# Optimization experiments

Measured on AMD Instinct MI355X. Metric: run time of the kernel, lower is better.

Reference implementation:

```python
import jax, jax.numpy as jnp
import numpy as np

B = 1024
EMB_DIM = 128      # channels fed to VQ; each channel's 5*5=25 spatial vector is one token
CODEBOOK = 1024
COMMIT = 0.25


def conv2d(x, w, b, pad=1):
    y = jax.lax.conv_general_dilated(x, w, (1, 1), [(pad, pad), (pad, pad)],
                                     dimension_numbers=('NCHW', 'OIHW', 'NCHW'))
    return y + b[None, :, None, None]


def maxpool2x2(x):
    b, c, h, w = x.shape
    xr = x.reshape(b, c, h // 2, 2, w // 2, 2).transpose(0, 1, 2, 4, 3, 5).reshape(b, c, h // 2, w // 2, 4)
    return jnp.max(xr, axis=-1), jnp.argmax(xr, axis=-1)


def maxunpool2x2(x, idx):
    b, c, h, w = x.shape
    y = x[..., None] * jax.nn.one_hot(idx, 4, dtype=x.dtype)
    return y.reshape(b, c, h, w, 2, 2).transpose(0, 1, 2, 4, 3, 5).reshape(b, c, h * 2, w * 2)


def setup_inputs() -> dict:
    key = jax.random.key(0)
    ks = jax.random.split(key, 12)
    f32 = jnp.float32

    def he(k, shape, fan_in):
        return jax.random.normal(k, shape, f32) * (2.0 / fan_in) ** 0.5

    return {
        'x': jax.random.normal(ks[0], (B, 3, 20, 20), f32),
        'enc1_w': he(ks[1], (32, 3, 3, 3), 27), 'enc1_b': jnp.zeros((32,), f32),
        'enc2_w': he(ks[2], (96, 32, 3, 3), 288), 'enc2_b': jnp.zeros((96,), f32),
        'pre_w': he(ks[3], (EMB_DIM, 96, 1, 1), 96), 'pre_b': jnp.zeros((EMB_DIM,), f32),
        'codebook': jax.random.normal(ks[4], (CODEBOOK, 25), f32),
        'trans_w': he(ks[5], (EMB_DIM, 96, 1, 1), EMB_DIM), 'trans_b': jnp.zeros((96,), f32),
        'dec1_w': he(ks[6], (32, 96, 3, 3), 864), 'dec1_b': jnp.zeros((32,), f32),
        'dec2_w': he(ks[7], (3, 32, 3, 3), 288), 'dec2_b': jnp.zeros((3,), f32),
        'hpe_w1': he(ks[8], (2400, 32), 2400), 'hpe_b1': jnp.zeros((32,), f32),
        'hpe_w2': he(ks[9], (32, 36), 32), 'hpe_b2': jnp.zeros((36,), f32),
    }


def reference(x, enc1_w, enc1_b, enc2_w, enc2_b, pre_w, pre_b, codebook,
              trans_w, trans_b, dec1_w, dec1_b, dec2_w, dec2_b,
              hpe_w1, hpe_b1, hpe_w2, hpe_b2):
    bsz = x.shape[0]
    # ---- Encoder: conv+relu+pool x2, keeping pool argmax indices ----
    h1 = jax.nn.relu(conv2d(x, enc1_w, enc1_b))          # [B,32,20,20]
    p1, idx1 = maxpool2x2(h1)                            # [B,32,10,10]
    h2 = jax.nn.relu(conv2d(p1, enc2_w, enc2_b))         # [B,96,10,10]
    z, idx2 = maxpool2x2(h2)                             # [B,96,5,5]
    # ---- pre-VQ 1x1 conv, tokens are per-channel 25-dim spatial vectors ----
    vq = conv2d(z, pre_w, pre_b, pad=0).reshape(bsz, -1, 25)   # [B,EMB_DIM,25]
    flat = vq.reshape(-1, 25)
    # squared L2 distances to codebook, argmin quantization
    d = (jnp.sum(flat * flat, -1, keepdims=True)
         - 2.0 * flat @ codebook.T
         + jnp.sum(codebook * codebook, -1))             # [B*EMB_DIM, CODEBOOK]
    indices = jnp.argmin(d, axis=-1).reshape(bsz, -1)    # [B,EMB_DIM]
    quantized = codebook[indices]                        # [B,EMB_DIM,25] gather
    vq_loss = COMMIT * jnp.mean((jax.lax.stop_gradient(quantized) - vq) ** 2)
    # unreliable_mode == 2 -> noisy_indices = indices (identity path)
    z_rec = codebook[indices].reshape(bsz, -1, 5, 5)     # [B,EMB_DIM,5,5]
    # ---- ConvTranspose2d 1x1 (torch weight layout [in,out,1,1]) ----
    latent = jnp.einsum('bihw,io->bohw', z_rec, trans_w[:, :, 0, 0]) + trans_b[None, :, None, None]
    # ---- Decoder: unpool(idx2)+conv+relu, unpool(idx1)+conv ----
    u2 = maxunpool2x2(latent, idx2)                      # [B,96,10,10]
    d1 = jax.nn.relu(conv2d(u2, dec1_w, dec1_b))         # [B,32,10,10]
    u1 = maxunpool2x2(d1, idx1)                          # [B,32,20,20]
    r_x = conv2d(u1, dec2_w, dec2_b)                     # [B,3,20,20]
    # ---- pose head on flattened latent (2400 = 96*5*5) ----
    feat = latent.reshape(bsz, -1)
    kp = jax.nn.relu(feat @ hpe_w1 + hpe_b1) @ hpe_w2 + hpe_b2
    return vq_loss, r_x, kp.reshape(bsz, -1, 2)
```

## Files before the change

kernel.cpp:

```cpp
#include <hip/hip_runtime.h>

typedef unsigned char u8;
typedef unsigned long long u64;
typedef _Float16 h2 __attribute__((ext_vector_type(2)));

__device__ inline h2 h2bits(unsigned int u) { union { unsigned int u; h2 h; } c; c.u = u; return c.h; }
__device__ inline unsigned int bitsh2(h2 h) { union { unsigned int u; h2 h; } c; c.h = h; return c.u; }
__device__ inline unsigned int f2hbits(float v) {
    union { _Float16 h; unsigned short u; } c; c.h = (_Float16)v; return (unsigned int)c.u;
}

#if __has_builtin(__builtin_amdgcn_fdot2)
__device__ inline float fdot2(h2 a, h2 b, float c) { return __builtin_amdgcn_fdot2(a, b, c, false); }
#else
__device__ inline float fdot2(h2 a, h2 b, float c) {
    return c + (float)a.x * (float)b.x + (float)a.y * (float)b.y;
}
#endif

__global__ __launch_bounds__(256) void k0t(const float* __restrict__ cb,
                                           float* __restrict__ cnorm,
                                           float* __restrict__ lossacc,
                                           const float* __restrict__ e2w,
                                           float* __restrict__ wT2,
                                           const float* __restrict__ d1w,
                                           unsigned int* __restrict__ wH6u) {
    int g = blockIdx.x * 256 + threadIdx.x;
    if (g < 1024) {
        float s = 0.f;
#pragma unroll
        for (int d = 0; d < 25; ++d) { float v = cb[g * 25 + d]; s += v * v; }
        cnorm[g] = s;
    }
    if (g == 0) lossacc[0] = 0.f;
    for (int i = g; i < 27648; i += 8192) {
        int oc = i / 288, r = i % 288, ci = r / 9, k = r % 9;
        wT2[((ci * 3 + k / 3) * 96 + oc) * 3 + (k % 3)] = e2w[i];
    }
    for (int i = g; i < 13824; i += 8192) {
        int oc = i & 31, r = i >> 5;
        int kx = r % 3, r2 = r / 3, ky = r2 % 3, cp = r2 / 3;
        float a = d1w[(oc * 96 + 2 * cp) * 9 + ky * 3 + kx];
        float b = d1w[(oc * 96 + 2 * cp + 1) * 9 + ky * 3 + kx];
        h2 v; v.x = (_Float16)a; v.y = (_Float16)b;
        wH6u[i] = bitsh2(v);
    }
}

__global__ __launch_bounds__(128) void k1_enc1(const float* __restrict__ x,
                                               const float* __restrict__ w,
                                               const float* __restrict__ bias,
                                               float* __restrict__ p1,
                                               u64* __restrict__ idx1p) {
    const int img = blockIdx.x;
    const int tid = threadIdx.x;
    __shared__ __align__(16) float xs[1320];
    __shared__ float wss[864];
    __shared__ float bss[32];
    for (int i = tid; i < 1320; i += 128) xs[i] = 0.f;
    for (int i = tid; i < 864; i += 128) wss[i] = w[i];
    if (tid < 32) bss[tid] = bias[tid];
    __syncthreads();
    for (int i = tid; i < 1200; i += 128) {
        int ci = i / 400, s = i % 400, y = s / 20, xx = s % 20;
        xs[ci * 440 + y * 22 + xx + 1] = x[img * 1200 + i];
    }
    __syncthreads();
    if (tid >= 100) return;
    const int r = tid / 10, c = tid % 10;
    int ry[4]; bool mv[4];
#pragma unroll
    for (int wy = 0; wy < 4; ++wy) {
        int yy = 2 * r - 1 + wy;
        mv[wy] = (yy >= 0) && (yy <= 19);
        ry[wy] = min(max(yy, 0), 19);
    }
    u64 idxbits = 0;
    for (int ocg = 0; ocg < 4; ++ocg) {
        float acc[8][4];
#pragma unroll
        for (int j = 0; j < 8; ++j) {
            float bb = bss[ocg * 8 + j];
#pragma unroll
            for (int q = 0; q < 4; ++q) acc[j][q] = bb;
        }
        for (int ci = 0; ci < 3; ++ci) {
            float win[4][4];
#pragma unroll
            for (int wy = 0; wy < 4; ++wy)
#pragma unroll
                for (int wx = 0; wx < 4; ++wx) {
                    float v = xs[ci * 440 + ry[wy] * 22 + 2 * c + wx];
                    win[wy][wx] = mv[wy] ? v : 0.f;
                }
#pragma unroll
            for (int j = 0; j < 8; ++j) {
                const float* wr = &wss[((ocg * 8 + j) * 3 + ci) * 9];
#pragma unroll
                for (int q = 0; q < 4; ++q) {
                    int dr = q >> 1, dc = q & 1;
#pragma unroll
                    for (int ky = 0; ky < 3; ++ky)
#pragma unroll
                        for (int kx = 0; kx < 3; ++kx)
                            acc[j][q] = fmaf(win[dr + ky][dc + kx], wr[ky * 3 + kx], acc[j][q]);
                }
            }
        }
#pragma unroll
        for (int j = 0; j < 8; ++j) {
            int oc = ocg * 8 + j;
            float best = -1.f; int bi = 0;
#pragma unroll
            for (int q = 0; q < 4; ++q) {
                float v = fmaxf(acc[j][q], 0.f);
                if (v > best) { best = v; bi = q; }
            }
            p1[img * 3200 + oc * 100 + tid] = best;
            idxbits |= (u64)bi << (2 * oc);
        }
    }
    idx1p[img * 100 + tid] = idxbits;
}

__global__ __launch_bounds__(256) void k2_enc2(const float* __restrict__ p1,
                                               const float* __restrict__ wT2,
                                               const float* __restrict__ bias,
                                               float* __restrict__ z_g,
                                               u8* __restrict__ idx2) {
    const int img = blockIdx.x;
    const int tid = threadIdx.x;
    __shared__ __align__(16) float up[4608];
    __shared__ __align__(16) float wch[6912];
    for (int i = tid; i < 4608; i += 256) up[i] = 0.f;
    __syncthreads();
    for (int i = tid; i < 3200; i += 256) {
        int ci = i / 100, s = i % 100;
        up[ci * 144 + (s / 10 + 1) * 12 + (s % 10) + 1] = p1[img * 3200 + i];
    }
    const int wv = tid >> 6;
    const int l  = tid & 63;
    const int ocsub = (l >= 25) ? 1 : 0;
    const int pos = l - ocsub * 25;
    const bool act = (l < 50);
    const int oc0 = wv * 24 + ocsub * 12;
    const int r = pos / 5, c = pos % 5;
    float acc[12][4];
#pragma unroll
    for (int j = 0; j < 12; ++j)
#pragma unroll
        for (int q = 0; q < 4; ++q) acc[j][q] = 0.f;
    for (int chunk = 0; chunk < 4; ++chunk) {
        __syncthreads();
        for (int i = tid; i < 6912; i += 256) wch[i] = wT2[chunk * 6912 + i];
        __syncthreads();
        if (act) {
            for (int cil = 0; cil < 8; ++cil) {
                const int base = (chunk * 8 + cil) * 144;
                float win[4][4];
#pragma unroll
                for (int wy = 0; wy < 4; ++wy) {
                    float2 a = *(const float2*)&up[base + (2 * r + wy) * 12 + 2 * c];
                    float2 b = *(const float2*)&up[base + (2 * r + wy) * 12 + 2 * c + 2];
                    win[wy][0] = a.x; win[wy][1] = a.y; win[wy][2] = b.x; win[wy][3] = b.y;
                }
#pragma unroll
                for (int ky = 0; ky < 3; ++ky) {
                    const float* wk = &wch[(cil * 3 + ky) * 288 + oc0 * 3];
                    float wreg[36];
#pragma unroll
                    for (int i4 = 0; i4 < 9; ++i4)
                        *(float4*)(wreg + 4 * i4) = *(const float4*)(wk + 4 * i4);
#pragma unroll
                    for (int j = 0; j < 12; ++j)
#pragma unroll
                        for (int q = 0; q < 4; ++q) {
                            int dr = q >> 1, dc = q & 1;
#pragma unroll
                            for (int kx = 0; kx < 3; ++kx)
                                acc[j][q] = fmaf(win[dr + ky][dc + kx], wreg[j * 3 + kx], acc[j][q]);
                        }
                }
            }
        }
    }
    if (act) {
#pragma unroll
        for (int j = 0; j < 12; ++j) {
            int oc = oc0 + j;
            float bb = bias[oc];
            float best = -1.f; int bi = 0;
#pragma unroll
            for (int q = 0; q < 4; ++q) {
                float v = fmaxf(acc[j][q] + bb, 0.f);
                if (v > best) { best = v; bi = q; }
            }
            z_g[img * 2400 + oc * 25 + pos] = best;
            idx2[img * 2400 + oc * 25 + pos] = (u8)bi;
        }
    }
}

__global__ __launch_bounds__(128) void k3a_pre(const float* __restrict__ z_g,
                                               const float* __restrict__ w,
                                               const float* __restrict__ bias,
                                               float* __restrict__ vqb) {
    const int img = blockIdx.x;
    const int tid = threadIdx.x;
    __shared__ __align__(16) float zs[2688];
    __shared__ float ob[3200];
    for (int i = tid; i < 2688; i += 128) zs[i] = 0.f;
    __syncthreads();
    for (int i = tid; i < 2400; i += 128)
        zs[(i / 25) * 28 + (i % 25)] = z_g[img * 2400 + i];
    __syncthreads();
    float acc[25];
    {
        float bbv = bias[tid];
#pragma unroll
        for (int s = 0; s < 25; ++s) acc[s] = bbv;
    }
    const float4* w4 = (const float4*)(w + tid * 96);
    for (int c4 = 0; c4 < 24; ++c4) {
        float4 wv = w4[c4];
        const int ci = c4 * 4;
#pragma unroll
        for (int u = 0; u < 4; ++u) {
            float wvu = (u == 0) ? wv.x : (u == 1) ? wv.y : (u == 2) ? wv.z : wv.w;
            float cz[28];
#pragma unroll
            for (int i = 0; i < 7; ++i)
                *(float4*)(cz + 4 * i) = *(const float4*)(&zs[(ci + u) * 28 + 4 * i]);
#pragma unroll
            for (int s = 0; s < 25; ++s) acc[s] = fmaf(wvu, cz[s], acc[s]);
        }
    }
#pragma unroll
    for (int s = 0; s < 25; ++s) ob[tid * 25 + s] = acc[s];
    __syncthreads();
    for (int i = tid; i < 3200; i += 128) vqb[img * 3200 + i] = ob[i];
}

__global__ __launch_bounds__(256) void k3b_vq2(const float* __restrict__ vq,
                                               const float* __restrict__ cb,
                                               const float* __restrict__ cnorm,
                                               float* __restrict__ pbest,
                                               int* __restrict__ pbk) {
    const int tg = blockIdx.x >> 3;
    const int ch = blockIdx.x & 7;
    const int tid = threadIdx.x;
    const int k0 = ch * 128;
    __shared__ __align__(16) float cs[128 * 28];
    for (int i = tid; i < 128 * 28; i += 256) {
        int k = i / 28, d = i % 28;
        float v = 0.f;
        if (d < 25) v = cb[(k0 + k) * 25 + d];
        else if (d == 25) v = cnorm[k0 + k];
        cs[i] = v;
    }
    const int t0 = tg * 1024 + tid * 4;
    float f2[4][25];
#pragma unroll
    for (int t = 0; t < 4; ++t)
#pragma unroll
        for (int d = 0; d < 25; ++d)
            f2[t][d] = -2.f * vq[(t0 + t) * 25 + d];
    __syncthreads();
    float best[4] = {1e30f, 1e30f, 1e30f, 1e30f};
    int bk[4] = {0, 0, 0, 0};
    for (int k = 0; k < 128; ++k) {
        const float* crow = &cs[k * 28];
        float cc[28];
#pragma unroll
        for (int i = 0; i < 7; ++i)
            *(float4*)(cc + 4 * i) = *(const float4*)(crow + 4 * i);
        const float cn = cc[25];
        const int kg = k0 + k;
#pragma unroll
        for (int t = 0; t < 4; ++t) {
            float a = cn;
#pragma unroll
            for (int d = 0; d < 25; ++d) a = fmaf(f2[t][d], cc[d], a);
            if (a < best[t]) { best[t] = a; bk[t] = kg; }
        }
    }
#pragma unroll
    for (int t = 0; t < 4; ++t) {
        pbest[ch * 131072 + t0 + t] = best[t];
        pbk[ch * 131072 + t0 + t] = bk[t];
    }
}

__global__ __launch_bounds__(256) void k3r_reduce(const float* __restrict__ pbest,
                                                  const int* __restrict__ pbk,
                                                  const float* __restrict__ vq,
                                                  int* __restrict__ vqidx,
                                                  float* __restrict__ lossacc) {
    const int t = blockIdx.x * 256 + threadIdx.x;
    float best = 1e30f; int bk = 0;
#pragma unroll
    for (int ch = 0; ch < 8; ++ch) {
        float s = pbest[ch * 131072 + t];
        int k = pbk[ch * 131072 + t];
        if (s < best) { best = s; bk = k; }
    }
    vqidx[t] = bk;
    float fn = 0.f;
#pragma unroll
    for (int d = 0; d < 25; ++d) { float v = vq[t * 25 + d]; fn = fmaf(v, v, fn); }
    float dloc = fn + best;
#pragma unroll
    for (int off = 32; off > 0; off >>= 1) dloc += __shfl_down(dloc, off, 64);
    __shared__ float wsum[4];
    if ((threadIdx.x & 63) == 0) wsum[threadIdx.x >> 6] = dloc;
    __syncthreads();
    if (threadIdx.x == 0)
        atomicAdd(lossacc, wsum[0] + wsum[1] + wsum[2] + wsum[3]);
}

__global__ void kf_loss(const float* __restrict__ lossacc, float* __restrict__ out) {
    out[0] = 0.25f * lossacc[0] / 3276800.0f;
}

__global__ __launch_bounds__(256) void k5_latent_pose(
    const int* __restrict__ vqidx, const float* __restrict__ cb,
    const float* __restrict__ tw, const float* __restrict__ tbb,
    const float* __restrict__ w1, const float* __restrict__ b1,
    const float* __restrict__ w2, const float* __restrict__ b2,
    float* __restrict__ latg, float* __restrict__ outkp) {
    const int img = blockIdx.x;
    const int tid = threadIdx.x;
    __shared__ int idxs[128];
    __shared__ float zr[128 * 26];
    __shared__ float lat[2400];
    __shared__ float ps[256];
    __shared__ float hs[32];
    if (tid < 128) idxs[tid] = vqidx[img * 128 + tid];
    __syncthreads();
    for (int i = tid; i < 3200; i += 256) {
        int e = i / 25, d = i % 25;
        zr[e * 26 + d] = cb[idxs[e] * 25 + d];
    }
    __syncthreads();
    const int sg = tid % 5, og = tid / 5;
    if (og < 24) {
        const int oc0 = og * 4, s0 = sg * 5;
        float acc[4][5];
#pragma unroll
        for (int j = 0; j < 4; ++j)
#pragma unroll
            for (int ss = 0; ss < 5; ++ss) acc[j][ss] = 0.f;
        for (int e = 0; e < 128; ++e) {
            float zv[5];
#pragma unroll
            for (int ss = 0; ss < 5; ++ss) zv[ss] = zr[e * 26 + s0 + ss];
#pragma unroll
            for (int j = 0; j < 4; ++j) {
                float wv = tw[e * 96 + oc0 + j];
#pragma unroll
                for (int ss = 0; ss < 5; ++ss) acc[j][ss] += wv * zv[ss];
            }
        }
#pragma unroll
        for (int j = 0; j < 4; ++j) {
            float bb = tbb[oc0 + j];
#pragma unroll
            for (int ss = 0; ss < 5; ++ss) {
                float v = acc[j][ss] + bb;
                lat[(oc0 + j) * 25 + s0 + ss] = v;
                latg[img * 2400 + (oc0 + j) * 25 + s0 + ss] = v;
            }
        }
    }
    __syncthreads();
    {
        const int seg = tid >> 5, jj = tid & 31;
        float s = 0.f;
        const int i0 = seg * 300;
        for (int i = i0; i < i0 + 300; ++i) s += lat[i] * w1[i * 32 + jj];
        ps[seg * 32 + jj] = s;
    }
    __syncthreads();
    if (tid < 32) {
        float h = b1[tid];
#pragma unroll
        for (int s2 = 0; s2 < 8; ++s2) h += ps[s2 * 32 + tid];
        hs[tid] = fmaxf(h, 0.f);
    }
    __syncthreads();
    if (tid < 36) {
        float kp = b2[tid];
#pragma unroll
        for (int m = 0; m < 32; ++m) kp += hs[m] * w2[m * 36 + tid];
        outkp[img * 36 + tid] = kp;
    }
}

__global__ __launch_bounds__(128) void k6_dec1(const float* __restrict__ latg,
                                               const u8* __restrict__ idx2,
                                               const unsigned int* __restrict__ wH6,
                                               const float* __restrict__ bias,
                                               float* __restrict__ d1p) {
    const int img0 = blockIdx.x * 2;
    const int tid = threadIdx.x;
    __shared__ __align__(16) unsigned int uph[13824];
    __shared__ unsigned int wcs[2304];
    for (int i = tid; i < 13824; i += 128) uph[i] = 0u;
    __syncthreads();
    for (int g = tid; g < 2400; g += 128) {
        int m = g / 1200, r2 = g % 1200;
        int cp = r2 / 25, s = r2 % 25;
        int rr = (img0 + m) * 2400 + cp * 50 + s;
        int q0 = idx2[rr], q1 = idx2[rr + 25];
        float v0 = latg[rr], v1 = latg[rr + 25];
        unsigned int wq[4] = {0u, 0u, 0u, 0u};
        wq[q0] |= f2hbits(v0);
        wq[q1] |= f2hbits(v1) << 16;
        int pr = s / 5, pc = s % 5;
        int wb = m * 6912 + (cp * 12 + 2 * pr + 1) * 12 + 2 * pc + 1;
        uph[wb]      = wq[0];
        uph[wb + 1]  = wq[1];
        uph[wb + 12] = wq[2];
        uph[wb + 13] = wq[3];
    }
    const int m = tid >> 6;
    const int l = tid & 63;
    const int oc = l & 31, ys = l >> 5;
    float acc[50];
#pragma unroll
    for (int i = 0; i < 50; ++i) acc[i] = 0.f;
    for (int chunk = 0; chunk < 6; ++chunk) {
        __syncthreads();
        for (int i = tid; i < 2304; i += 128) wcs[i] = wH6[chunk * 2304 + i];
        __syncthreads();
        for (int cpl = 0; cpl < 8; ++cpl) {
            const int base = m * 6912 + (chunk * 8 + cpl) * 144 + ys * 60;
            unsigned int row[7][12];
#pragma unroll
            for (int k = 0; k < 7; ++k) {
                const uint4* rp = (const uint4*)&uph[base + k * 12];
                uint4 a = rp[0], b = rp[1], cc = rp[2];
                row[k][0] = a.x;  row[k][1] = a.y;  row[k][2] = a.z;  row[k][3] = a.w;
                row[k][4] = b.x;  row[k][5] = b.y;  row[k][6] = b.z;  row[k][7] = b.w;
                row[k][8] = cc.x; row[k][9] = cc.y; row[k][10] = cc.z; row[k][11] = cc.w;
            }
            h2 w9[9];
#pragma unroll
            for (int t = 0; t < 9; ++t) w9[t] = h2bits(wcs[(cpl * 9 + t) * 32 + oc]);
#pragma unroll
            for (int r = 0; r < 5; ++r)
#pragma unroll
                for (int j = 0; j < 10; ++j) {
                    float a = acc[r * 10 + j];
#pragma unroll
                    for (int ky = 0; ky < 3; ++ky)
#pragma unroll
                        for (int kx = 0; kx < 3; ++kx)
                            a = fdot2(h2bits(row[r + ky][j + kx]), w9[ky * 3 + kx], a);
                    acc[r * 10 + j] = a;
                }
        }
    }
    const float bb = bias[oc];
#pragma unroll
    for (int r = 0; r < 5; ++r)
#pragma unroll
        for (int j = 0; j < 10; ++j)
            d1p[(img0 + m) * 3200 + ((ys * 5 + r) * 10 + j) * 32 + oc] =
                fmaxf(acc[r * 10 + j] + bb, 0.f);
}

__global__ __launch_bounds__(256) void k7_dec2(const float* __restrict__ d1p,
                                               const u64* __restrict__ idx1p,
                                               const float* __restrict__ w,
                                               const float* __restrict__ bias,
                                               float* __restrict__ rx) {
    const int img = blockIdx.x;
    const int tid = threadIdx.x;
    __shared__ __align__(16) float up[14080];
    __shared__ float wss[864];
    __shared__ float bss[3];
    for (int i = tid; i < 14080; i += 256) up[i] = 0.f;
    for (int i = tid; i < 864; i += 256) wss[i] = w[i];
    if (tid < 3) bss[tid] = bias[tid];
    __syncthreads();
    for (int i = tid; i < 3200; i += 256) {
        int pos = i >> 5, ci = i & 31;
        int r = pos / 10, c = pos % 10;
        int q = (int)((idx1p[img * 100 + pos] >> (2 * ci)) & 3ull);
        up[ci * 440 + (2 * r + (q >> 1)) * 22 + 2 * c + (q & 1) + 1] = d1p[img * 3200 + i];
    }
    __syncthreads();
    if (tid >= 200) return;
    const int y = tid / 10, xp = tid % 10, x0 = 2 * xp;
    const bool m0 = (y > 0), m2 = (y < 19);
    const int ry0 = max(y - 1, 0), ry2 = min(y + 1, 19);
    float acc[3][2] = {{0.f, 0.f}, {0.f, 0.f}, {0.f, 0.f}};
    for (int ci = 0; ci < 32; ++ci) {
        const int base = ci * 440;
        float u[3][4];
        {
            float2 a0 = *(const float2*)&up[base + ry0 * 22 + x0];
            float2 a1 = *(const float2*)&up[base + ry0 * 22 + x0 + 2];
            u[0][0] = m0 ? a0.x : 0.f; u[0][1] = m0 ? a0.y : 0.f;
            u[0][2] = m0 ? a1.x : 0.f; u[0][3] = m0 ? a1.y : 0.f;
            float2 b0 = *(const float2*)&up[base + y * 22 + x0];
            float2 b1 = *(const float2*)&up[base + y * 22 + x0 + 2];
            u[1][0] = b0.x; u[1][1] = b0.y; u[1][2] = b1.x; u[1][3] = b1.y;
            float2 c0 = *(const float2*)&up[base + ry2 * 22 + x0];
            float2 c1 = *(const float2*)&up[base + ry2 * 22 + x0 + 2];
            u[2][0] = m2 ? c0.x : 0.f; u[2][1] = m2 ? c0.y : 0.f;
            u[2][2] = m2 ? c1.x : 0.f; u[2][3] = m2 ? c1.y : 0.f;
        }
#pragma unroll
        for (int oc = 0; oc < 3; ++oc) {
            const float* wr = &wss[(oc * 32 + ci) * 9];
#pragma unroll
            for (int dx = 0; dx < 2; ++dx)
#pragma unroll
                for (int ky = 0; ky < 3; ++ky)
#pragma unroll
                    for (int kx = 0; kx < 3; ++kx)
                        acc[oc][dx] = fmaf(u[ky][kx + dx], wr[ky * 3 + kx], acc[oc][dx]);
        }
    }
#pragma unroll
    for (int oc = 0; oc < 3; ++oc)
#pragma unroll
        for (int dx = 0; dx < 2; ++dx)
            rx[img * 1200 + oc * 400 + y * 20 + x0 + dx] = acc[oc][dx] + bss[oc];
}

extern "C" void kernel_launch(void* const* d_in, const int* in_sizes, int n_in,
                              void* d_out, int out_size, void* d_ws, size_t ws_size,
                              hipStream_t stream) {
    const float* x   = (const float*)d_in[0];
    const float* e1w = (const float*)d_in[1];
    const float* e1b = (const float*)d_in[2];
    const float* e2w = (const float*)d_in[3];
    const float* e2b = (const float*)d_in[4];
    const float* prw = (const float*)d_in[5];
    const float* prb = (const float*)d_in[6];
    const float* cb  = (const float*)d_in[7];
    const float* tw  = (const float*)d_in[8];
    const float* tbb = (const float*)d_in[9];
    const float* d1w = (const float*)d_in[10];
    const float* d1b = (const float*)d_in[11];
    const float* d2w = (const float*)d_in[12];
    const float* d2b = (const float*)d_in[13];
    const float* hw1 = (const float*)d_in[14];
    const float* hb1 = (const float*)d_in[15];
    const float* hw2 = (const float*)d_in[16];
    const float* hb2 = (const float*)d_in[17];
    float* out = (float*)d_out;

    float* ws      = (float*)d_ws;
    float* cnorm   = ws;
    float* lossacc = cnorm + 1024;
    float* wT2     = lossacc + 4;
    unsigned int* wH6u = (unsigned int*)(wT2 + 27648);
    float* p1      = wT2 + 27648 + 27648;
    float* z       = p1 + 3276800;
    float* vq      = z + 2457600;
    int*   vqidx   = (int*)(vq + 3276800);
    u64*   idx1p   = (u64*)(vqidx + 131072);
    u8*    idx2    = (u8*)(idx1p + 102400);
    float* latent  = p1;
    float* d1buf   = vq;
    float* pbest   = z;
    int*   pbk     = (int*)(z + 1048576);

    float* rx  = out + 1;
    float* okp = out + 1 + 1228800;

    k0t<<<32, 256, 0, stream>>>(cb, cnorm, lossacc, e2w, wT2, d1w, wH6u);
    k1_enc1<<<1024, 128, 0, stream>>>(x, e1w, e1b, p1, idx1p);
    k2_enc2<<<1024, 256, 0, stream>>>(p1, wT2, e2b, z, idx2);
    k3a_pre<<<1024, 128, 0, stream>>>(z, prw, prb, vq);
    k3b_vq2<<<1024, 256, 0, stream>>>(vq, cb, cnorm, pbest, pbk);
    k3r_reduce<<<512, 256, 0, stream>>>(pbest, pbk, vq, vqidx, lossacc);
    kf_loss<<<1, 1, 0, stream>>>(lossacc, out);
    k5_latent_pose<<<1024, 256, 0, stream>>>(vqidx, cb, tw, tbb, hw1, hb1, hw2, hb2,
                                             latent, okp);
    k6_dec1<<<512, 128, 0, stream>>>(latent, idx2, wH6u, d1b, d1buf);
    k7_dec2<<<1024, 256, 0, stream>>>(d1buf, idx1p, d2w, d2b, rx);
}
```

Before: 470.8 us.

## Fuse pre-VQ 1x1 conv into enc2 and use fp16 packed dot in dec2

Merges the 1x1 pre-quantization conv into the enc2 kernel, so the pooled activations stay in shared memory instead of being written to and re-read from global memory, and one launch is dropped. Separately, dec1 now writes its output as fp16, and dec2 unpools packed half2 channel pairs and accumulates with fdot2 using weights pre-packed to fp16 in the setup kernel. This halves the intermediate traffic and the dec2 inner-loop instruction count. The cost is fp16 rounding in the decoder's last conv and more shared-memory reuse and barriers in the fused encoder kernel.

```diff
diff --git a/kernel.cpp b/kernel.cpp
--- a/kernel.cpp
+++ b/kernel.cpp
@@ -24,7 +24,9 @@
                                            const float* __restrict__ e2w,
                                            float* __restrict__ wT2,
                                            const float* __restrict__ d1w,
-                                           unsigned int* __restrict__ wH6u) {
+                                           unsigned int* __restrict__ wH6u,
+                                           const float* __restrict__ d2w,
+                                           unsigned int* __restrict__ wH7u) {
     int g = blockIdx.x * 256 + threadIdx.x;
     if (g < 1024) {
         float s = 0.f;
@@ -44,6 +46,14 @@
         float b = d1w[(oc * 96 + 2 * cp + 1) * 9 + ky * 3 + kx];
         h2 v; v.x = (_Float16)a; v.y = (_Float16)b;
         wH6u[i] = bitsh2(v);
+    }
+    if (g < 432) {
+        int oc = g % 3, r = g / 3;
+        int kx = r % 3, r2 = r / 3, ky = r2 % 3, cp = r2 / 3;
+        float a = d2w[(oc * 32 + 2 * cp) * 9 + ky * 3 + kx];
+        float b = d2w[(oc * 32 + 2 * cp + 1) * 9 + ky * 3 + kx];
+        h2 v; v.x = (_Float16)a; v.y = (_Float16)b;
+        wH7u[g] = bitsh2(v);
     }
 }
 
@@ -123,11 +133,13 @@
     idx1p[img * 100 + tid] = idxbits;
 }
 
-__global__ __launch_bounds__(256) void k2_enc2(const float* __restrict__ p1,
-                                               const float* __restrict__ wT2,
-                                               const float* __restrict__ bias,
-                                               float* __restrict__ z_g,
-                                               u8* __restrict__ idx2) {
+__global__ __launch_bounds__(256) void k2f(const float* __restrict__ p1,
+                                           const float* __restrict__ wT2,
+                                           const float* __restrict__ bias,
+                                           const float* __restrict__ prw,
+                                           const float* __restrict__ prb,
+                                           float* __restrict__ vqb,
+                                           u8* __restrict__ idx2) {
     const int img = blockIdx.x;
     const int tid = threadIdx.x;
     __shared__ __align__(16) float up[4608];
@@ -184,6 +196,9 @@
             }
         }
     }
+    float* zs = wch;
+    float* wst = &wch[2688];
+    __syncthreads();
     if (act) {
 #pragma unroll
         for (int j = 0; j < 12; ++j) {
@@ -195,50 +210,41 @@
                 float v = fmaxf(acc[j][q] + bb, 0.f);
                 if (v > best) { best = v; bi = q; }
             }
-            z_g[img * 2400 + oc * 25 + pos] = best;
+            zs[oc * 28 + pos] = best;
             idx2[img * 2400 + oc * 25 + pos] = (u8)bi;
         }
     }
-}
-
-__global__ __launch_bounds__(128) void k3a_pre(const float* __restrict__ z_g,
-                                               const float* __restrict__ w,
-                                               const float* __restrict__ bias,
-                                               float* __restrict__ vqb) {
-    const int img = blockIdx.x;
-    const int tid = threadIdx.x;
-    __shared__ __align__(16) float zs[2688];
-    __shared__ float ob[3200];
-    for (int i = tid; i < 2688; i += 128) zs[i] = 0.f;
-    __syncthreads();
-    for (int i = tid; i < 2400; i += 128)
-        zs[(i / 25) * 28 + (i % 25)] = z_g[img * 2400 + i];
-    __syncthreads();
-    float acc[25];
+    __syncthreads();
+    const int e = tid >> 1, sh = tid & 1;
+    const int s0 = sh * 12, ns = sh ? 13 : 12;
+    float acc2[13];
     {
-        float bbv = bias[tid];
-#pragma unroll
-        for (int s = 0; s < 25; ++s) acc[s] = bbv;
-    }
-    const float4* w4 = (const float4*)(w + tid * 96);
-    for (int c4 = 0; c4 < 24; ++c4) {
-        float4 wv = w4[c4];
-        const int ci = c4 * 4;
-#pragma unroll
-        for (int u = 0; u < 4; ++u) {
-            float wvu = (u == 0) ? wv.x : (u == 1) ? wv.y : (u == 2) ? wv.z : wv.w;
-            float cz[28];
-#pragma unroll
-            for (int i = 0; i < 7; ++i)
-                *(float4*)(cz + 4 * i) = *(const float4*)(&zs[(ci + u) * 28 + 4 * i]);
-#pragma unroll
-            for (int s = 0; s < 25; ++s) acc[s] = fmaf(wvu, cz[s], acc[s]);
-        }
-    }
-#pragma unroll
-    for (int s = 0; s < 25; ++s) ob[tid * 25 + s] = acc[s];
-    __syncthreads();
-    for (int i = tid; i < 3200; i += 128) vqb[img * 3200 + i] = ob[i];
+        float bb = prb[e];
+#pragma unroll
+        for (int k = 0; k < 13; ++k) acc2[k] = bb;
+    }
+    for (int cc = 0; cc < 3; ++cc) {
+        __syncthreads();
+        for (int i = tid; i < 4096; i += 256)
+            wst[(i >> 5) * 33 + (i & 31)] = prw[(i >> 5) * 96 + cc * 32 + (i & 31)];
+        __syncthreads();
+        for (int cil = 0; cil < 32; ++cil) {
+            int ci = cc * 32 + cil;
+            float wvv = wst[e * 33 + cil];
+            float cz[16];
+#pragma unroll
+            for (int i4 = 0; i4 < 4; ++i4)
+                *(float4*)(cz + 4 * i4) = *(const float4*)&zs[ci * 28 + s0 + 4 * i4];
+#pragma unroll
+            for (int k = 0; k < 13; ++k) acc2[k] = fmaf(wvv, cz[k], acc2[k]);
+        }
+    }
+    float* ob = up;
+#pragma unroll
+    for (int k = 0; k < 13; ++k)
+        if (k < ns) ob[e * 25 + s0 + k] = acc2[k];
+    __syncthreads();
+    for (int i = tid; i < 3200; i += 256) vqb[img * 3200 + i] = ob[i];
 }
 
 __global__ __launch_bounds__(256) void k3b_vq2(const float* __restrict__ vq,
@@ -400,7 +406,7 @@
                                                const u8* __restrict__ idx2,
                                                const unsigned int* __restrict__ wH6,
                                                const float* __restrict__ bias,
-                                               float* __restrict__ d1p) {
+                                               unsigned short* __restrict__ d1h) {
     const int img0 = blockIdx.x * 2;
     const int tid = threadIdx.x;
     __shared__ __align__(16) unsigned int uph[13824];
@@ -466,29 +472,40 @@
     for (int r = 0; r < 5; ++r)
 #pragma unroll
         for (int j = 0; j < 10; ++j)
-            d1p[(img0 + m) * 3200 + ((ys * 5 + r) * 10 + j) * 32 + oc] =
-                fmaxf(acc[r * 10 + j] + bb, 0.f);
-}
-
-__global__ __launch_bounds__(256) void k7_dec2(const float* __restrict__ d1p,
+            d1h[(img0 + m) * 3200 + ((ys * 5 + r) * 10 + j) * 32 + oc] =
+                (unsigned short)f2hbits(fmaxf(acc[r * 10 + j] + bb, 0.f));
+}
+
+__global__ __launch_bounds__(256) void k7_dec2(const unsigned int* __restrict__ d1w32,
                                                const u64* __restrict__ idx1p,
-                                               const float* __restrict__ w,
+                                               const unsigned int* __restrict__ wH7,
                                                const float* __restrict__ bias,
                                                float* __restrict__ rx) {
     const int img = blockIdx.x;
     const int tid = threadIdx.x;
-    __shared__ __align__(16) float up[14080];
-    __shared__ float wss[864];
-    __shared__ float bss[3];
-    for (int i = tid; i < 14080; i += 256) up[i] = 0.f;
-    for (int i = tid; i < 864; i += 256) wss[i] = w[i];
-    if (tid < 3) bss[tid] = bias[tid];
-    __syncthreads();
-    for (int i = tid; i < 3200; i += 256) {
-        int pos = i >> 5, ci = i & 31;
+    __shared__ __align__(16) unsigned int uph[7040];
+    __shared__ unsigned int wcs[448];
+    for (int i = tid; i < 7040; i += 256) uph[i] = 0u;
+    for (int i = tid; i < 448; i += 256) {
+        int cp = i / 28, rr = i % 28;
+        wcs[i] = (rr < 27) ? wH7[cp * 27 + rr] : 0u;
+    }
+    __syncthreads();
+    for (int g = tid; g < 1600; g += 256) {
+        int pos = g >> 4, cp = g & 15;
+        unsigned int word = d1w32[img * 1600 + g];
+        u64 bits = idx1p[img * 100 + pos];
+        int q0 = (int)((bits >> (4 * cp)) & 3ull);
+        int q1 = (int)((bits >> (4 * cp + 2)) & 3ull);
+        unsigned int wq[4] = {0u, 0u, 0u, 0u};
+        wq[q0] |= word & 0xFFFFu;
+        wq[q1] |= word & 0xFFFF0000u;
         int r = pos / 10, c = pos % 10;
-        int q = (int)((idx1p[img * 100 + pos] >> (2 * ci)) & 3ull);
-        up[ci * 440 + (2 * r + (q >> 1)) * 22 + 2 * c + (q & 1) + 1] = d1p[img * 3200 + i];
+        int wb = cp * 440 + (2 * r) * 22 + 2 * c + 1;
+        uph[wb]      = wq[0];
+        uph[wb + 1]  = wq[1];
+        uph[wb + 22] = wq[2];
+        uph[wb + 23] = wq[3];
     }
     __syncthreads();
     if (tid >= 200) return;
@@ -496,39 +513,38 @@
     const bool m0 = (y > 0), m2 = (y < 19);
     const int ry0 = max(y - 1, 0), ry2 = min(y + 1, 19);
     float acc[3][2] = {{0.f, 0.f}, {0.f, 0.f}, {0.f, 0.f}};
-    for (int ci = 0; ci < 32; ++ci) {
-        const int base = ci * 440;
-        float u[3][4];
+    for (int cp = 0; cp < 16; ++cp) {
+        const int base = cp * 440;
+        unsigned int row[3][4];
         {
-            float2 a0 = *(const float2*)&up[base + ry0 * 22 + x0];
-            float2 a1 = *(const float2*)&up[base + ry0 * 22 + x0 + 2];
-            u[0][0] = m0 ? a0.x : 0.f; u[0][1] = m0 ? a0.y : 0.f;
-            u[0][2] = m0 ? a1.x : 0.f; u[0][3] = m0 ? a1.y : 0.f;
-            float2 b0 = *(const float2*)&up[base + y * 22 + x0];
-            float2 b1 = *(const float2*)&up[base + y * 22 + x0 + 2];
-            u[1][0] = b0.x; u[1][1] = b0.y; u[1][2] = b1.x; u[1][3] = b1.y;
-            float2 c0 = *(const float2*)&up[base + ry2 * 22 + x0];
-            float2 c1 = *(const float2*)&up[base + ry2 * 22 + x0 + 2];
-            u[2][0] = m2 ? c0.x : 0.f; u[2][1] = m2 ? c0.y : 0.f;
-            u[2][2] = m2 ? c1.x : 0.f; u[2][3] = m2 ? c1.y : 0.f;
-        }
-#pragma unroll
-        for (int oc = 0; oc < 3; ++oc) {
-            const float* wr = &wss[(oc * 32 + ci) * 9];
-#pragma unroll
-            for (int dx = 0; dx < 2; ++dx)
-#pragma unroll
-                for (int ky = 0; ky < 3; ++ky)
-#pragma unroll
-                    for (int kx = 0; kx < 3; ++kx)
-                        acc[oc][dx] = fmaf(u[ky][kx + dx], wr[ky * 3 + kx], acc[oc][dx]);
-        }
+            uint2 a = *(const uint2*)&uph[base + ry0 * 22 + x0];
+            uint2 b = *(const uint2*)&uph[base + ry0 * 22 + x0 + 2];
+            row[0][0] = m0 ? a.x : 0u; row[0][1] = m0 ? a.y : 0u;
+            row[0][2] = m0 ? b.x : 0u; row[0][3] = m0 ? b.y : 0u;
+            a = *(const uint2*)&uph[base + y * 22 + x0];
+            b = *(const uint2*)&uph[base + y * 22 + x0 + 2];
+            row[1][0] = a.x; row[1][1] = a.y; row[1][2] = b.x; row[1][3] = b.y;
+            a = *(const uint2*)&uph[base + ry2 * 22 + x0];
+            b = *(const uint2*)&uph[base + ry2 * 22 + x0 + 2];
+            row[2][0] = m2 ? a.x : 0u; row[2][1] = m2 ? a.y : 0u;
+            row[2][2] = m2 ? b.x : 0u; row[2][3] = m2 ? b.y : 0u;
+        }
+#pragma unroll
+        for (int oc = 0; oc < 3; ++oc)
+#pragma unroll
+            for (int ky = 0; ky < 3; ++ky)
+#pragma unroll
+                for (int kx = 0; kx < 3; ++kx) {
+                    h2 wk = h2bits(wcs[cp * 28 + (ky * 3 + kx) * 3 + oc]);
+                    acc[oc][0] = fdot2(h2bits(row[ky][kx]),     wk, acc[oc][0]);
+                    acc[oc][1] = fdot2(h2bits(row[ky][kx + 1]), wk, acc[oc][1]);
+                }
     }
 #pragma unroll
     for (int oc = 0; oc < 3; ++oc)
 #pragma unroll
         for (int dx = 0; dx < 2; ++dx)
-            rx[img * 1200 + oc * 400 + y * 20 + x0 + dx] = acc[oc][dx] + bss[oc];
+            rx[img * 1200 + oc * 400 + y * 20 + x0 + dx] = acc[oc][dx] + bias[oc];
 }
 
 extern "C" void kernel_launch(void* const* d_in, const int* in_sizes, int n_in,
@@ -559,6 +575,7 @@
     float* lossacc = cnorm + 1024;
     float* wT2     = lossacc + 4;
     unsigned int* wH6u = (unsigned int*)(wT2 + 27648);
+    unsigned int* wH7u = wH6u + 13824;
     float* p1      = wT2 + 27648 + 27648;
     float* z       = p1 + 3276800;
     float* vq      = z + 2457600;
@@ -566,22 +583,21 @@
     u64*   idx1p   = (u64*)(vqidx + 131072);
     u8*    idx2    = (u8*)(idx1p + 102400);
     float* latent  = p1;
-    float* d1buf   = vq;
+    unsigned short* d1h = (unsigned short*)vq;
     float* pbest   = z;
     int*   pbk     = (int*)(z + 1048576);
 
     float* rx  = out + 1;
     float* okp = out + 1 + 1228800;
 
-    k0t<<<32, 256, 0, stream>>>(cb, cnorm, lossacc, e2w, wT2, d1w, wH6u);
+    k0t<<<32, 256, 0, stream>>>(cb, cnorm, lossacc, e2w, wT2, d1w, wH6u, d2w, wH7u);
     k1_enc1<<<1024, 128, 0, stream>>>(x, e1w, e1b, p1, idx1p);
-    k2_enc2<<<1024, 256, 0, stream>>>(p1, wT2, e2b, z, idx2);
-    k3a_pre<<<1024, 128, 0, stream>>>(z, prw, prb, vq);
+    k2f<<<1024, 256, 0, stream>>>(p1, wT2, e2b, prw, prb, vq, idx2);
     k3b_vq2<<<1024, 256, 0, stream>>>(vq, cb, cnorm, pbest, pbk);
     k3r_reduce<<<512, 256, 0, stream>>>(pbest, pbk, vq, vqidx, lossacc);
     kf_loss<<<1, 1, 0, stream>>>(lossacc, out);
     k5_latent_pose<<<1024, 256, 0, stream>>>(vqidx, cb, tw, tbb, hw1, hb1, hw2, hb2,
                                              latent, okp);
-    k6_dec1<<<512, 128, 0, stream>>>(latent, idx2, wH6u, d1b, d1buf);
-    k7_dec2<<<1024, 256, 0, stream>>>(d1buf, idx1p, d2w, d2b, rx);
-}
+    k6_dec1<<<512, 128, 0, stream>>>(latent, idx2, wH6u, d1b, d1h);
+    k7_dec2<<<1024, 256, 0, stream>>>((const unsigned int*)d1h, idx1p, wH7u, d2b, rx);
+}
```

Measured after the change: 443.7 us, median of 3. -5.7%, faster.
